# Optimization experiments

Hardware: AMD Instinct MI355X
Metric: run time of the kernel (lower is better)

## Reference

```python
import jax, jax.numpy as jnp
import numpy as np

N, E = 40000, 640000
NODE_DIM, EDGE_DIM, H = 128, 64, 8
DK = NODE_DIM // H


def setup_inputs() -> dict:
    key = jax.random.key(0)
    ks = jax.random.split(key, 12)
    s = 1.0 / np.sqrt(NODE_DIM)
    se = 1.0 / np.sqrt(EDGE_DIM)
    return {
        "nodes": jax.random.normal(ks[0], (N, NODE_DIM), jnp.float32),
        "edge_index": jax.random.randint(ks[1], (2, E), 0, N, jnp.int64),
        "edge_attr": jax.random.normal(ks[2], (E, EDGE_DIM), jnp.float32),
        # Linear weights stored as [in, out] so y = x @ W + b
        "wq": jax.random.uniform(ks[3], (NODE_DIM, NODE_DIM), jnp.float32, -s, s),
        "bq": jnp.zeros((NODE_DIM,), jnp.float32),
        "wk": jax.random.uniform(ks[4], (NODE_DIM, NODE_DIM), jnp.float32, -s, s),
        "bk": jnp.zeros((NODE_DIM,), jnp.float32),
        "wv": jax.random.uniform(ks[5], (NODE_DIM, NODE_DIM), jnp.float32, -s, s),
        "bv": jnp.zeros((NODE_DIM,), jnp.float32),
        "we": jax.random.uniform(ks[6], (EDGE_DIM, NODE_DIM), jnp.float32, -se, se),
        "be": jnp.zeros((NODE_DIM,), jnp.float32),
        "wo": jax.random.uniform(ks[7], (NODE_DIM, NODE_DIM), jnp.float32, -s, s),
        "bo": jnp.zeros((NODE_DIM,), jnp.float32),
    }


def reference(nodes, edge_index, edge_attr, wq, bq, wk, bk, wv, bv, we, be, wo, bo):
    n = nodes.shape[0]
    inv_sqrt_dk = 1.0 / np.sqrt(DK).astype(np.float32)
    Q = (nodes @ wq + bq).reshape(n, H, DK)
    K = (nodes @ wk + bk).reshape(n, H, DK)
    V = (nodes @ wv + bv).reshape(n, H, DK)
    row, col = edge_index[0], edge_index[1]
    Qr = Q[row]                                   # [E, H, DK]
    scores = (Qr * K[col]).sum(-1) * inv_sqrt_dk  # [E, H]
    ef = (edge_attr @ we + be).reshape(-1, H, DK)
    scores = scores + (Qr * ef).sum(-1) * inv_sqrt_dk
    es = jnp.exp(scores)                          # unnormalized exp (matches torch code: no max-subtraction)
    denom = jax.ops.segment_sum(es, row, num_segments=n)       # [N, H]
    w = es / (denom[row] + 1e-8)                  # [E, H]
    msg = w[..., None] * V[col]                   # [E, H, DK]
    out = jax.ops.segment_sum(msg, row, num_segments=n).reshape(n, -1)
    return out @ wo + bo
```

## Files before the change

### kernel.cpp

```cpp
#include <hip/hip_runtime.h>
#include <hip/hip_fp16.h>

#define NN  40000
#define NE  640000
#define ND  128
#define ED  64
#define NH  8
#define DK  16
#define NWT 912

#define SCAN_NBLK 157
#define PREP_NBLK 524
#define GEMM1_NBLK 625

typedef _Float16 f16x8 __attribute__((ext_vector_type(8)));
typedef float    f32x4 __attribute__((ext_vector_type(4)));

__global__ __launch_bounds__(256) void k_prep_hist(const float* __restrict__ wq,
                                                   const float* __restrict__ bq,
                                                   const float* __restrict__ wk,
                                                   const float* __restrict__ bk,
                                                   const float* __restrict__ wv,
                                                   const float* __restrict__ bv,
                                                   const float* __restrict__ we,
                                                   const float* __restrict__ be,
                                                   const float* __restrict__ wo,
                                                   const int* __restrict__ ei,
                                                   __half* __restrict__ WT,
                                                   __half* __restrict__ woT,
                                                   float* __restrict__ bias_all,
                                                   int* __restrict__ hist) {
  if (blockIdx.x >= PREP_NBLK) {
    const int e = (blockIdx.x - PREP_NBLK) * 256 + threadIdx.x;
    if (e < NE) atomicAdd(&hist[ei[e]], 1);
    return;
  }
  int idx = blockIdx.x * 256 + threadIdx.x;
  if (idx < NWT * ND) {
    const int n = idx >> 7, k = idx & 127;
    float v;
    if (n < 128)      v = wq[k * ND + n];
    else if (n < 256) v = wk[k * ND + (n - 128)];
    else if (n < 384) v = wv[k * ND + (n - 256)];
    else if (n < 896) {
      const int col = n - 384, h = col >> 6, j = col & 63;
      const float4* a = (const float4*)(wq + (size_t)k * ND + h * DK);
      const float4* b = (const float4*)(we + (size_t)j * ND + h * DK);
      float s = 0.f;
#pragma unroll
      for (int i = 0; i < 4; ++i) {
        float4 av = a[i], bv4 = b[i];
        s = fmaf(av.x, bv4.x, s); s = fmaf(av.y, bv4.y, s);
        s = fmaf(av.z, bv4.z, s); s = fmaf(av.w, bv4.w, s);
      }
      v = 0.25f * s;
    } else if (n < 904) {
      const int h = n - 896;
      const float4* a = (const float4*)(wq + (size_t)k * ND + h * DK);
      const float4* b = (const float4*)(be + h * DK);
      float s = 0.f;
#pragma unroll
      for (int i = 0; i < 4; ++i) {
        float4 av = a[i], bv4 = b[i];
        s = fmaf(av.x, bv4.x, s); s = fmaf(av.y, bv4.y, s);
        s = fmaf(av.z, bv4.z, s); s = fmaf(av.w, bv4.w, s);
      }
      v = 0.25f * s;
    } else v = 0.f;
    WT[idx] = __float2half_rn(v);
    return;
  }
  idx -= NWT * ND;
  if (idx < ND * ND) {
    const int n = idx >> 7, k = idx & 127;
    woT[idx] = __float2half_rn(wo[k * ND + n]);
    return;
  }
  idx -= ND * ND;
  if (idx < NWT) {
    float v;
    if (idx < 128)      v = bq[idx];
    else if (idx < 256) v = bk[idx - 128];
    else if (idx < 384) v = bv[idx - 256];
    else if (idx < 896) {
      const int col = idx - 384, h = col >> 6, j = col & 63;
      const float4* a = (const float4*)(bq + h * DK);
      const float4* b = (const float4*)(we + (size_t)j * ND + h * DK);
      float s = 0.f;
#pragma unroll
      for (int i = 0; i < 4; ++i) {
        float4 av = a[i], bv4 = b[i];
        s = fmaf(av.x, bv4.x, s); s = fmaf(av.y, bv4.y, s);
        s = fmaf(av.z, bv4.z, s); s = fmaf(av.w, bv4.w, s);
      }
      v = 0.25f * s;
    } else if (idx < 904) {
      const int h = idx - 896;
      const float4* a = (const float4*)(bq + h * DK);
      const float4* b = (const float4*)(be + h * DK);
      float s = 0.f;
#pragma unroll
      for (int i = 0; i < 4; ++i) {
        float4 av = a[i], bv4 = b[i];
        s = fmaf(av.x, bv4.x, s); s = fmaf(av.y, bv4.y, s);
        s = fmaf(av.z, bv4.z, s); s = fmaf(av.w, bv4.w, s);
      }
      v = 0.25f * s;
    } else v = 0.f;
    bias_all[idx] = v;
  }
}

__global__ __launch_bounds__(256) void k_scan_fused(const int* __restrict__ hist,
                                                    int* __restrict__ off,
                                                    int* __restrict__ cursor,
                                                    int* __restrict__ pub) {
  __shared__ int sh[256];
  const int tid = threadIdx.x;
  const int b = blockIdx.x;
  const int idx = b * 256 + tid;
  const int v = (idx < NN) ? hist[idx] : 0;
  sh[tid] = v;
  __syncthreads();
#pragma unroll
  for (int d = 1; d < 256; d <<= 1) {
    int t = (tid >= d) ? sh[tid - d] : 0;
    __syncthreads();
    sh[tid] += t;
    __syncthreads();
  }
  const int incl = sh[tid];
  const int total = sh[255];

  if (tid == 0) atomicExch(&pub[b], total + 1);

  int contrib = 0;
  if (tid < b) {
    int vv;
    do { vv = atomicAdd(&pub[tid], 0); } while (vv == 0);
    contrib = vv - 1;
  }
  __syncthreads();
  sh[tid] = contrib;
  __syncthreads();
#pragma unroll
  for (int d = 128; d > 0; d >>= 1) {
    if (tid < d) sh[tid] += sh[tid + d];
    __syncthreads();
  }
  const int excl = incl - v + sh[0];
  if (idx < NN) {
    off[idx] = excl;
    cursor[idx] = excl;
  }
  if (b == 0 && tid == 0) off[NN] = NE;
}

__global__ __launch_bounds__(256) void k_gemm1_scatter(const float* __restrict__ x,
                                                       const __half* __restrict__ WT,
                                                       const float* __restrict__ bias_all,
                                                       const int* __restrict__ ei,
                                                       int* __restrict__ cursor,
                                                       int2* __restrict__ pair,
                                                       __half* __restrict__ qh,
                                                       __half* __restrict__ K16,
                                                       __half* __restrict__ V16,
                                                       __half* __restrict__ G16,
                                                       float* __restrict__ SB) {
  __shared__ _Float16 bs[4][16][132];

  if (blockIdx.x >= GEMM1_NBLK) {
    const int e = (blockIdx.x - GEMM1_NBLK) * 256 + threadIdx.x;
    if (e < NE) {
      const int row = ei[e];
      const int col = ei[NE + e];
      const int pos = atomicAdd(&cursor[row], 1);
      pair[pos] = make_int2(col, e);
    }
    return;
  }

  const int wave = threadIdx.x >> 6;
  const int l    = threadIdx.x & 63;
  const int row  = l & 15;
  const int kq   = l >> 4;
  const int r0   = blockIdx.x * 64 + wave * 16;

  f16x8 a[4];
#pragma unroll
  for (int s = 0; s < 4; ++s) {
    const float4* ap = (const float4*)(x + (size_t)(r0 + row) * ND + s * 32 + kq * 8);
    const float4 f0 = ap[0], f1 = ap[1];
    f16x8 t;
    t[0] = (_Float16)f0.x; t[1] = (_Float16)f0.y; t[2] = (_Float16)f0.z; t[3] = (_Float16)f0.w;
    t[4] = (_Float16)f1.x; t[5] = (_Float16)f1.y; t[6] = (_Float16)f1.z; t[7] = (_Float16)f1.w;
    a[s] = t;
  }

  const int rb = r0 + kq * 4;

  for (int nc = 0; nc < 56; nc += 4) {
    __syncthreads();
    {
      const __half* src = WT + (size_t)((nc + wave) * 16 + row) * ND;
      _Float16* dst = &bs[wave][row][0];
#pragma unroll
      for (int ch = 0; ch < 4; ++ch) {
        const int o = (kq + ch * 4) * 8;
        *(f16x8*)(dst + o) = *(const f16x8*)(src + o);
      }
    }
    __syncthreads();
#pragma unroll
    for (int t = 0; t < 4; ++t) {
      const int nt = nc + t;
      f32x4 c = {0.f, 0.f, 0.f, 0.f};
#pragma unroll
      for (int s = 0; s < 4; ++s) {
        const f16x8 b = *(const f16x8*)&bs[t][row][s * 32 + kq * 8];
        c = __builtin_amdgcn_mfma_f32_16x16x32_f16(a[s], b, c, 0, 0, 0);
      }
      const int col = nt * 16 + row;
      const float bb = bias_all[col];
      if (nt < 24) {
        __half* dst = (nt < 8) ? (qh + col) : (nt < 16) ? (K16 + (col - 128)) : (V16 + (col - 256));
#pragma unroll
        for (int i = 0; i < 4; ++i)
          dst[(size_t)(rb + i) * ND] = __float2half_rn(c[i] + bb);
      } else {
        const int gcol = col - 384;
#pragma unroll
        for (int i = 0; i < 4; ++i)
          G16[(size_t)(rb + i) * 512 + gcol] = __float2half_rn(c[i] + bb);
      }
    }
  }

  {
    f32x4 c = {0.f, 0.f, 0.f, 0.f};
#pragma unroll
    for (int s = 0; s < 4; ++s) {
      const f16x8 b = *(const f16x8*)(WT + (size_t)(896 + row) * ND + s * 32 + kq * 8);
      c = __builtin_amdgcn_mfma_f32_16x16x32_f16(a[s], b, c, 0, 0, 0);
    }
    if (row < 8) {
      const float bb = bias_all[896 + row];
#pragma unroll
      for (int i = 0; i < 4; ++i)
        SB[(size_t)(rb + i) * NH + row] = c[i] + bb;
    }
  }
}

__global__ __launch_bounds__(256) void k_gemm2(const __half* __restrict__ mh,
                                               const __half* __restrict__ woT,
                                               const float* __restrict__ bo,
                                               float* __restrict__ out) {
  __shared__ _Float16 ws[128][132];
  const int tid  = threadIdx.x;
  const int wave = tid >> 6;
  const int l    = tid & 63;
  const int row  = l & 15;
  const int kq   = l >> 4;
  const int r0   = blockIdx.x * 64 + wave * 16;

  {
    const int r = tid & 127, hf = tid >> 7;
    const __half* src = woT + (size_t)r * ND + hf * 64;
    _Float16* dst = &ws[r][hf * 64];
#pragma unroll
    for (int ch = 0; ch < 8; ++ch)
      *(f16x8*)(dst + ch * 8) = *(const f16x8*)(src + ch * 8);
  }

  f16x8 a[4];
#pragma unroll
  for (int s = 0; s < 4; ++s)
    a[s] = *(const f16x8*)(mh + (size_t)(r0 + row) * ND + s * 32 + kq * 8);

  __syncthreads();

  const int rb = r0 + kq * 4;
#pragma unroll 2
  for (int nt = 0; nt < 8; ++nt) {
    f32x4 c = {0.f, 0.f, 0.f, 0.f};
#pragma unroll
    for (int s = 0; s < 4; ++s) {
      const f16x8 b = *(const f16x8*)&ws[nt * 16 + row][s * 32 + kq * 8];
      c = __builtin_amdgcn_mfma_f32_16x16x32_f16(a[s], b, c, 0, 0, 0);
    }
    const int col = nt * 16 + row;
    const float bb = bo[col];
#pragma unroll
    for (int i = 0; i < 4; ++i)
      out[(size_t)(rb + i) * ND + col] = c[i] + bb;
  }
}

__global__ __launch_bounds__(256) void k_gather(const __half* __restrict__ qh,
                                                const __half* __restrict__ K16,
                                                const __half* __restrict__ V16,
                                                const float* __restrict__ ea,
                                                const int* __restrict__ off,
                                                const int2* __restrict__ pair,
                                                const __half* __restrict__ G16,
                                                const float* __restrict__ SB,
                                                __half* __restrict__ mh) {
  __shared__ float eas[8][8 * ED];
  const int g = threadIdx.x >> 5;
  const int n = blockIdx.x * 8 + g;
  const int l = threadIdx.x & 31;
  const int h = l >> 2;
  const int q = l & 3;

  float gg[16];
  float4 qv;
  {
    const __half2* qp2 = (const __half2*)(qh + (size_t)n * ND + h * DK + q * 4);
    float2 q01 = __half22float2(qp2[0]);
    float2 q23 = __half22float2(qp2[1]);
    qv.x = q01.x * 0.25f; qv.y = q01.y * 0.25f;
    qv.z = q23.x * 0.25f; qv.w = q23.y * 0.25f;
  }
  const float sb = SB[n * NH + h];
  {
    const float4* gp = (const float4*)(G16 + (size_t)n * 512 + h * 64 + q * 16);
    float4 c0 = gp[0], c1 = gp[1];
    const __half2* h0 = (const __half2*)&c0;
    const __half2* h1 = (const __half2*)&c1;
#pragma unroll
    for (int i = 0; i < 4; ++i) {
      float2 f0 = __half22float2(h0[i]);
      gg[2 * i + 0] = f0.x; gg[2 * i + 1] = f0.y;
      float2 f1 = __half22float2(h1[i]);
      gg[8 + 2 * i + 0] = f1.x; gg[8 + 2 * i + 1] = f1.y;
    }
  }

  float4 acc = make_float4(0.f, 0.f, 0.f, 0.f);
  float den = 0.f;

  const int j0 = off[n], j1 = off[n + 1];
  const int jlast = j1 - 1;
  const int hq = h * DK + q * 4;
  const int l8 = l & 7;
  const int se = l >> 2;
  const int sp = l & 3;

  if (j0 < j1) {
    int2 p = pair[min(j0 + l8, jlast)];
    float4 er0, er1, er2, er3;
    {
      const int eid = __shfl(p.y, se, 32);
      const float4* s4 = (const float4*)(ea + (size_t)eid * ED) + sp;
      er0 = s4[0]; er1 = s4[4]; er2 = s4[8]; er3 = s4[12];
    }
    int2 pn = pair[min(j0 + 8 + l8, jlast)];

    for (int jp = j0; jp < j1; jp += 8) {
      int cols[8];
#pragma unroll
      for (int c = 0; c < 8; ++c) cols[c] = __shfl(p.x, c, 32);
      float2 kz[8], vz[8];
#pragma unroll
      for (int c = 0; c < 8; ++c) {
        kz[c] = *(const float2*)(K16 + (size_t)cols[c] * ND + hq);
        vz[c] = *(const float2*)(V16 + (size_t)cols[c] * ND + hq);
      }

      {
        float* d = &eas[g][se * ED] + sp * 4;
        *(float4*)(d + 0)  = er0; *(float4*)(d + 16) = er1;
        *(float4*)(d + 32) = er2; *(float4*)(d + 48) = er3;
      }
      int2 pf = pn;
      if (jp + 8 < j1) {
        const int eidN = __shfl(pn.y, se, 32);
        const float4* s4 = (const float4*)(ea + (size_t)eidN * ED) + sp;
        er0 = s4[0]; er1 = s4[4]; er2 = s4[8]; er3 = s4[12];
        pf = pair[min(jp + 16 + l8, jlast)];
      }

      asm volatile("s_waitcnt lgkmcnt(0)" ::: "memory");
      __builtin_amdgcn_sched_barrier(0);

      __builtin_amdgcn_s_setprio(1);
#pragma unroll
      for (int c = 0; c < 8; ++c) {
        const __half2* kh = (const __half2*)&kz[c];
        const float2 ka = __half22float2(kh[0]);
        const float2 kb = __half22float2(kh[1]);

        float s = ka.x * qv.x;
        s = fmaf(qv.y, ka.y, s); s = fmaf(qv.z, kb.x, s); s = fmaf(qv.w, kb.y, s);

        const float4* ep = (const float4*)&eas[g][c * ED + q * 16];
#pragma unroll
        for (int i = 0; i < 4; ++i) {
          float4 a = ep[i];
          s = fmaf(a.x, gg[4 * i + 0], s); s = fmaf(a.y, gg[4 * i + 1], s);
          s = fmaf(a.z, gg[4 * i + 2], s); s = fmaf(a.w, gg[4 * i + 3], s);
        }

        s += __shfl_xor(s, 1); s += __shfl_xor(s, 2);
        const float es = (jp + c < j1) ? __expf(s + sb) : 0.f;
        den += es;

        const __half2* vh = (const __half2*)&vz[c];
        const float2 va = __half22float2(vh[0]);
        const float2 vb = __half22float2(vh[1]);
        acc.x = fmaf(es, va.x, acc.x); acc.y = fmaf(es, va.y, acc.y);
        acc.z = fmaf(es, vb.x, acc.z); acc.w = fmaf(es, vb.y, acc.w);
      }
      __builtin_amdgcn_s_setprio(0);

      p = pn; pn = pf;
    }
  }

  const float inv = 1.f / (den + 1e-8f);
  union { __half2 h2[2]; float2 f; } u;
  u.h2[0] = __floats2half2_rn(acc.x * inv, acc.y * inv);
  u.h2[1] = __floats2half2_rn(acc.z * inv, acc.w * inv);
  *(float2*)(mh + (size_t)n * ND + h * DK + q * 4) = u.f;
}

extern "C" void kernel_launch(void* const* d_in, const int* in_sizes, int n_in,
                              void* d_out, int out_size, void* d_ws, size_t ws_size,
                              hipStream_t stream) {
  const float* nodes = (const float*)d_in[0];
  const int*   ei    = (const int*)d_in[1];
  const float* ea    = (const float*)d_in[2];
  const float* wq    = (const float*)d_in[3];
  const float* bq    = (const float*)d_in[4];
  const float* wk    = (const float*)d_in[5];
  const float* bk    = (const float*)d_in[6];
  const float* wv    = (const float*)d_in[7];
  const float* bv    = (const float*)d_in[8];
  const float* we    = (const float*)d_in[9];
  const float* be    = (const float*)d_in[10];
  const float* wo    = (const float*)d_in[11];
  const float* bo    = (const float*)d_in[12];
  float* out = (float*)d_out;

  const size_t NND = (size_t)NN * ND;
  __half* qh   = (__half*)d_ws;
  __half* K16  = qh + NND;
  __half* V16  = K16 + NND;
  __half* mh   = V16 + NND;
  __half* G16  = mh + NND;
  __half* WT   = G16 + (size_t)NN * 512;
  __half* woT  = WT + (size_t)NWT * ND;
  float* SB    = (float*)(woT + ND * ND);
  float* bias_all = SB + (size_t)NN * NH;
  int* hist    = (int*)(bias_all + NWT);
  int* pub     = hist + NN;
  int* off     = pub + 160;
  int* cursor  = off + 40004;
  int2* pair   = (int2*)(cursor + NN);

  hipMemsetAsync(hist, 0, (NN + 160) * sizeof(int), stream);

  dim3 blk(256);

  k_prep_hist<<<dim3(PREP_NBLK + (NE + 255) / 256), blk, 0, stream>>>(
      wq, bq, wk, bk, wv, bv, we, be, wo, ei, WT, woT, bias_all, hist);

  k_scan_fused<<<dim3(SCAN_NBLK), blk, 0, stream>>>(hist, off, cursor, pub);

  k_gemm1_scatter<<<dim3(GEMM1_NBLK + (NE + 255) / 256), blk, 0, stream>>>(
      nodes, WT, bias_all, ei, cursor, pair, qh, K16, V16, G16, SB);

  k_gather<<<dim3(NN / 8), blk, 0, stream>>>(qh, K16, V16, ea, off, pair, G16, SB, mh);

  k_gemm2<<<dim3(NN / 64), blk, 0, stream>>>(mh, woT, bo, out);
}
```

Baseline: 184.4 us.

## Pre-sort edge attributes to fp16 in CSR order during scatter, simplify gather

```diff
diff --git a/kernel.cpp b/kernel.cpp
--- a/kernel.cpp
+++ b/kernel.cpp
@@ -160,8 +160,10 @@
                                                        const __half* __restrict__ WT,
                                                        const float* __restrict__ bias_all,
                                                        const int* __restrict__ ei,
+                                                       const float* __restrict__ ea,
                                                        int* __restrict__ cursor,
-                                                       int2* __restrict__ pair,
+                                                       int* __restrict__ colA,
+                                                       __half* __restrict__ ea16,
                                                        __half* __restrict__ qh,
                                                        __half* __restrict__ K16,
                                                        __half* __restrict__ V16,
@@ -175,7 +177,19 @@
       const int row = ei[e];
       const int col = ei[NE + e];
       const int pos = atomicAdd(&cursor[row], 1);
-      pair[pos] = make_int2(col, e);
+      colA[pos] = col;
+      const float4* src = (const float4*)(ea + (size_t)e * ED);
+      __half* dst = ea16 + (size_t)pos * ED;
+#pragma unroll
+      for (int i = 0; i < 8; ++i) {
+        const float4 v0 = src[2 * i], v1 = src[2 * i + 1];
+        union { __half2 h[4]; float4 f; } u;
+        u.h[0] = __floats2half2_rn(v0.x, v0.y);
+        u.h[1] = __floats2half2_rn(v0.z, v0.w);
+        u.h[2] = __floats2half2_rn(v1.x, v1.y);
+        u.h[3] = __floats2half2_rn(v1.z, v1.w);
+        *(float4*)(dst + i * 8) = u.f;
+      }
     }
     return;
   }
@@ -300,20 +314,17 @@
 __global__ __launch_bounds__(256) void k_gather(const __half* __restrict__ qh,
                                                 const __half* __restrict__ K16,
                                                 const __half* __restrict__ V16,
-                                                const float* __restrict__ ea,
+                                                const __half* __restrict__ ea16,
                                                 const int* __restrict__ off,
-                                                const int2* __restrict__ pair,
+                                                const int* __restrict__ colA,
                                                 const __half* __restrict__ G16,
                                                 const float* __restrict__ SB,
                                                 __half* __restrict__ mh) {
-  __shared__ float eas[8][8 * ED];
-  const int g = threadIdx.x >> 5;
-  const int n = blockIdx.x * 8 + g;
+  const int n = blockIdx.x * 8 + (threadIdx.x >> 5);
   const int l = threadIdx.x & 31;
   const int h = l >> 2;
   const int q = l & 3;
 
-  float gg[16];
   float4 qv;
   {
     const __half2* qp2 = (const __half2*)(qh + (size_t)n * ND + h * DK + q * 4);
@@ -323,18 +334,14 @@
     qv.z = q23.x * 0.25f; qv.w = q23.y * 0.25f;
   }
   const float sb = SB[n * NH + h];
+  __half2 gg2[8];
   {
     const float4* gp = (const float4*)(G16 + (size_t)n * 512 + h * 64 + q * 16);
     float4 c0 = gp[0], c1 = gp[1];
-    const __half2* h0 = (const __half2*)&c0;
-    const __half2* h1 = (const __half2*)&c1;
-#pragma unroll
-    for (int i = 0; i < 4; ++i) {
-      float2 f0 = __half22float2(h0[i]);
-      gg[2 * i + 0] = f0.x; gg[2 * i + 1] = f0.y;
-      float2 f1 = __half22float2(h1[i]);
-      gg[8 + 2 * i + 0] = f1.x; gg[8 + 2 * i + 1] = f1.y;
-    }
+    const __half2* p0 = (const __half2*)&c0;
+    const __half2* p1 = (const __half2*)&c1;
+#pragma unroll
+    for (int i = 0; i < 4; ++i) { gg2[i] = p0[i]; gg2[4 + i] = p1[i]; }
   }
 
   float4 acc = make_float4(0.f, 0.f, 0.f, 0.f);
@@ -344,78 +351,56 @@
   const int jlast = j1 - 1;
   const int hq = h * DK + q * 4;
   const int l8 = l & 7;
-  const int se = l >> 2;
-  const int sp = l & 3;
-
-  if (j0 < j1) {
-    int2 p = pair[min(j0 + l8, jlast)];
-    float4 er0, er1, er2, er3;
-    {
-      const int eid = __shfl(p.y, se, 32);
-      const float4* s4 = (const float4*)(ea + (size_t)eid * ED) + sp;
-      er0 = s4[0]; er1 = s4[4]; er2 = s4[8]; er3 = s4[12];
-    }
-    int2 pn = pair[min(j0 + 8 + l8, jlast)];
-
-    for (int jp = j0; jp < j1; jp += 8) {
-      int cols[8];
-#pragma unroll
-      for (int c = 0; c < 8; ++c) cols[c] = __shfl(p.x, c, 32);
-      float2 kz[8], vz[8];
-#pragma unroll
-      for (int c = 0; c < 8; ++c) {
-        kz[c] = *(const float2*)(K16 + (size_t)cols[c] * ND + hq);
-        vz[c] = *(const float2*)(V16 + (size_t)cols[c] * ND + hq);
-      }
-
-      {
-        float* d = &eas[g][se * ED] + sp * 4;
-        *(float4*)(d + 0)  = er0; *(float4*)(d + 16) = er1;
-        *(float4*)(d + 32) = er2; *(float4*)(d + 48) = er3;
-      }
-      int2 pf = pn;
-      if (jp + 8 < j1) {
-        const int eidN = __shfl(pn.y, se, 32);
-        const float4* s4 = (const float4*)(ea + (size_t)eidN * ED) + sp;
-        er0 = s4[0]; er1 = s4[4]; er2 = s4[8]; er3 = s4[12];
-        pf = pair[min(jp + 16 + l8, jlast)];
-      }
-
-      asm volatile("s_waitcnt lgkmcnt(0)" ::: "memory");
-      __builtin_amdgcn_sched_barrier(0);
-
-      __builtin_amdgcn_s_setprio(1);
-#pragma unroll
-      for (int c = 0; c < 8; ++c) {
-        const __half2* kh = (const __half2*)&kz[c];
-        const float2 ka = __half22float2(kh[0]);
-        const float2 kb = __half22float2(kh[1]);
-
-        float s = ka.x * qv.x;
-        s = fmaf(qv.y, ka.y, s); s = fmaf(qv.z, kb.x, s); s = fmaf(qv.w, kb.y, s);
-
-        const float4* ep = (const float4*)&eas[g][c * ED + q * 16];
-#pragma unroll
-        for (int i = 0; i < 4; ++i) {
-          float4 a = ep[i];
-          s = fmaf(a.x, gg[4 * i + 0], s); s = fmaf(a.y, gg[4 * i + 1], s);
-          s = fmaf(a.z, gg[4 * i + 2], s); s = fmaf(a.w, gg[4 * i + 3], s);
-        }
-
-        s += __shfl_xor(s, 1); s += __shfl_xor(s, 2);
-        const float es = (jp + c < j1) ? __expf(s + sb) : 0.f;
-        den += es;
-
-        const __half2* vh = (const __half2*)&vz[c];
-        const float2 va = __half22float2(vh[0]);
-        const float2 vb = __half22float2(vh[1]);
-        acc.x = fmaf(es, va.x, acc.x); acc.y = fmaf(es, va.y, acc.y);
-        acc.z = fmaf(es, vb.x, acc.z); acc.w = fmaf(es, vb.y, acc.w);
-      }
-      __builtin_amdgcn_s_setprio(0);
-
-      p = pn; pn = pf;
-    }
+  const __half2 hzero = __float2half2_rn(0.f);
+
+  for (int jp = j0; jp < j1; jp += 8) {
+    const int cv = colA[min(jp + l8, jlast)];
+    int cols[8];
+#pragma unroll
+    for (int c = 0; c < 8; ++c) cols[c] = __shfl(cv, c, 32);
+
+    float2 kz[8], vz[8];
+#pragma unroll
+    for (int c = 0; c < 8; ++c) {
+      kz[c] = *(const float2*)(K16 + (size_t)cols[c] * ND + hq);
+      vz[c] = *(const float2*)(V16 + (size_t)cols[c] * ND + hq);
+    }
+
+    __builtin_amdgcn_s_setprio(1);
+#pragma unroll
+    for (int c = 0; c < 8; ++c) {
+      const __half2* kh = (const __half2*)&kz[c];
+      const float2 ka = __half22float2(kh[0]);
+      const float2 kb = __half22float2(kh[1]);
+
+      float s = ka.x * qv.x;
+      s = fmaf(qv.y, ka.y, s); s = fmaf(qv.z, kb.x, s); s = fmaf(qv.w, kb.y, s);
+
+      const float4* ep = (const float4*)(ea16 + (size_t)min(jp + c, jlast) * ED + q * 16);
+      const float4 e0 = ep[0], e1 = ep[1];
+      const __half2* eh0 = (const __half2*)&e0;
+      const __half2* eh1 = (const __half2*)&e1;
+      __half2 hacc0 = hzero, hacc1 = hzero;
+#pragma unroll
+      for (int i = 0; i < 4; ++i) {
+        hacc0 = __hfma2(eh0[i], gg2[i], hacc0);
+        hacc1 = __hfma2(eh1[i], gg2[4 + i], hacc1);
+      }
+      const float2 f0 = __half22float2(hacc0);
+      const float2 f1 = __half22float2(hacc1);
+      s += (f0.x + f0.y) + (f1.x + f1.y);
+
+      s += __shfl_xor(s, 1); s += __shfl_xor(s, 2);
+      const float es = (jp + c < j1) ? __expf(s + sb) : 0.f;
+      den += es;
+
+      const __half2* vh = (const __half2*)&vz[c];
+      const float2 va = __half22float2(vh[0]);
+      const float2 vb = __half22float2(vh[1]);
+      acc.x = fmaf(es, va.x, acc.x); acc.y = fmaf(es, va.y, acc.y);
+      acc.z = fmaf(es, vb.x, acc.z); acc.w = fmaf(es, vb.y, acc.w);
+    }
+    __builtin_amdgcn_s_setprio(0);
   }
 
   const float inv = 1.f / (den + 1e-8f);
@@ -451,13 +436,14 @@
   __half* G16  = mh + NND;
   __half* WT   = G16 + (size_t)NN * 512;
   __half* woT  = WT + (size_t)NWT * ND;
-  float* SB    = (float*)(woT + ND * ND);
+  __half* ea16 = woT + (size_t)ND * ND;
+  float* SB    = (float*)(ea16 + (size_t)NE * ED);
   float* bias_all = SB + (size_t)NN * NH;
   int* hist    = (int*)(bias_all + NWT);
   int* pub     = hist + NN;
   int* off     = pub + 160;
   int* cursor  = off + 40004;
-  int2* pair   = (int2*)(cursor + NN);
+  int* colA    = cursor + NN;
 
   hipMemsetAsync(hist, 0, (NN + 160) * sizeof(int), stream);
 
@@ -469,9 +455,9 @@
   k_scan_fused<<<dim3(SCAN_NBLK), blk, 0, stream>>>(hist, off, cursor, pub);
 
   k_gemm1_scatter<<<dim3(GEMM1_NBLK + (NE + 255) / 256), blk, 0, stream>>>(
-      nodes, WT, bias_all, ei, cursor, pair, qh, K16, V16, G16, SB);
-
-  k_gather<<<dim3(NN / 8), blk, 0, stream>>>(qh, K16, V16, ea, off, pair, G16, SB, mh);
+      nodes, WT, bias_all, ei, ea, cursor, colA, ea16, qh, K16, V16, G16, SB);
+
+  k_gather<<<dim3(NN / 8), blk, 0, stream>>>(qh, K16, V16, ea16, off, colA, G16, SB, mh);
 
   k_gemm2<<<dim3(NN / 64), blk, 0, stream>>>(mh, woT, bo, out);
 }
```

After: 236.8 us. 1.28x slower.

## Sort nodes by degree so gather blocks process similar-length edge lists

Applied to the files above, without the earlier changes.

```diff
diff --git a/kernel.cpp b/kernel.cpp
--- a/kernel.cpp
+++ b/kernel.cpp
@@ -12,6 +12,7 @@
 #define SCAN_NBLK 157
 #define PREP_NBLK 524
 #define GEMM1_NBLK 625
+#define SCAT_NBLK 2500
 
 typedef _Float16 f16x8 __attribute__((ext_vector_type(8)));
 typedef float    f32x4 __attribute__((ext_vector_type(4)));
@@ -114,12 +115,14 @@
 __global__ __launch_bounds__(256) void k_scan_fused(const int* __restrict__ hist,
                                                     int* __restrict__ off,
                                                     int* __restrict__ cursor,
-                                                    int* __restrict__ pub) {
+                                                    int* __restrict__ pub,
+                                                    int* __restrict__ dh) {
   __shared__ int sh[256];
   const int tid = threadIdx.x;
   const int b = blockIdx.x;
   const int idx = b * 256 + tid;
   const int v = (idx < NN) ? hist[idx] : 0;
+  if (idx < NN) atomicAdd(&dh[min(v, 255)], 1);
   sh[tid] = v;
   __syncthreads();
 #pragma unroll
@@ -156,11 +159,31 @@
   if (b == 0 && tid == 0) off[NN] = NE;
 }
 
+__global__ __launch_bounds__(256) void k_dscan(const int* __restrict__ dh,
+                                               int* __restrict__ dcur) {
+  __shared__ int sh[256];
+  const int tid = threadIdx.x;
+  const int v = dh[tid];
+  sh[tid] = v;
+  __syncthreads();
+#pragma unroll
+  for (int d = 1; d < 256; d <<= 1) {
+    int t = (tid >= d) ? sh[tid - d] : 0;
+    __syncthreads();
+    sh[tid] += t;
+    __syncthreads();
+  }
+  dcur[tid] = sh[tid] - v;
+}
+
 __global__ __launch_bounds__(256) void k_gemm1_scatter(const float* __restrict__ x,
                                                        const __half* __restrict__ WT,
                                                        const float* __restrict__ bias_all,
                                                        const int* __restrict__ ei,
+                                                       const int* __restrict__ off,
                                                        int* __restrict__ cursor,
+                                                       int* __restrict__ dcur,
+                                                       int* __restrict__ perm,
                                                        int2* __restrict__ pair,
                                                        __half* __restrict__ qh,
                                                        __half* __restrict__ K16,
@@ -169,6 +192,15 @@
                                                        float* __restrict__ SB) {
   __shared__ _Float16 bs[4][16][132];
 
+  if (blockIdx.x >= GEMM1_NBLK + SCAT_NBLK) {
+    const int n = (blockIdx.x - GEMM1_NBLK - SCAT_NBLK) * 256 + threadIdx.x;
+    if (n < NN) {
+      const int d = min(off[n + 1] - off[n], 255);
+      const int pos = atomicAdd(&dcur[d], 1);
+      perm[pos] = n;
+    }
+    return;
+  }
   if (blockIdx.x >= GEMM1_NBLK) {
     const int e = (blockIdx.x - GEMM1_NBLK) * 256 + threadIdx.x;
     if (e < NE) {
@@ -305,10 +337,11 @@
                                                 const int2* __restrict__ pair,
                                                 const __half* __restrict__ G16,
                                                 const float* __restrict__ SB,
+                                                const int* __restrict__ perm,
                                                 __half* __restrict__ mh) {
   __shared__ float eas[8][8 * ED];
   const int g = threadIdx.x >> 5;
-  const int n = blockIdx.x * 8 + g;
+  const int n = perm[blockIdx.x * 8 + g];
   const int l = threadIdx.x & 31;
   const int h = l >> 2;
   const int q = l & 3;
@@ -455,23 +488,28 @@
   float* bias_all = SB + (size_t)NN * NH;
   int* hist    = (int*)(bias_all + NWT);
   int* pub     = hist + NN;
-  int* off     = pub + 160;
+  int* dh      = pub + 160;
+  int* dcur    = dh + 256;
+  int* off     = dcur + 256;
   int* cursor  = off + 40004;
-  int2* pair   = (int2*)(cursor + NN);
-
-  hipMemsetAsync(hist, 0, (NN + 160) * sizeof(int), stream);
+  int* perm    = cursor + NN;
+  int2* pair   = (int2*)(perm + NN);
+
+  hipMemsetAsync(hist, 0, (NN + 160 + 256) * sizeof(int), stream);
 
   dim3 blk(256);
 
   k_prep_hist<<<dim3(PREP_NBLK + (NE + 255) / 256), blk, 0, stream>>>(
       wq, bq, wk, bk, wv, bv, we, be, wo, ei, WT, woT, bias_all, hist);
 
-  k_scan_fused<<<dim3(SCAN_NBLK), blk, 0, stream>>>(hist, off, cursor, pub);
-
-  k_gemm1_scatter<<<dim3(GEMM1_NBLK + (NE + 255) / 256), blk, 0, stream>>>(
-      nodes, WT, bias_all, ei, cursor, pair, qh, K16, V16, G16, SB);
-
-  k_gather<<<dim3(NN / 8), blk, 0, stream>>>(qh, K16, V16, ea, off, pair, G16, SB, mh);
+  k_scan_fused<<<dim3(SCAN_NBLK), blk, 0, stream>>>(hist, off, cursor, pub, dh);
+
+  k_dscan<<<dim3(1), blk, 0, stream>>>(dh, dcur);
+
+  k_gemm1_scatter<<<dim3(GEMM1_NBLK + SCAT_NBLK + SCAN_NBLK), blk, 0, stream>>>(
+      nodes, WT, bias_all, ei, off, cursor, dcur, perm, pair, qh, K16, V16, G16, SB);
+
+  k_gather<<<dim3(NN / 8), blk, 0, stream>>>(qh, K16, V16, ea, off, pair, G16, SB, perm, mh);
 
   k_gemm2<<<dim3(NN / 64), blk, 0, stream>>>(mh, woT, bo, out);
 }
```

Result: slower. 353.1 us (+91.5%).
